# Kernel optimization log

Hardware: AMD Instinct MI355X
Metric: run time of the kernel (lower is better)

The kernel has to match this reference:

```python
import jax, jax.numpy as jnp
import numpy as np

N, T, D, H = 100000, 16, 8, 40
HP1 = H + 1
ALPHA_DP = 1.0
KAPPA0 = 1000.0   # priorGaussianVarKappa
NU0 = 100.0       # priorWishartNu
PSI0_SCALE = 500.0  # priorWishartPsi = 500*I


def setup_inputs() -> dict:
    key = jax.random.key(0)
    ks = jax.random.split(key, 6)
    return {
        "BetaGamma1": jnp.ones((1, T), jnp.float32),
        "Phi": jax.random.uniform(ks[0], (N, T), jnp.float32),
        "inputData": jax.random.normal(ks[1], (N, D), jnp.float32),
        "outputData": jax.random.normal(ks[2], (N, 1), jnp.float32),
        "weightELM": jax.random.uniform(ks[3], (D, H), jnp.float32) * 2.0 - 1.0,
        "biasELM": jax.random.normal(ks[4], (H, 1), jnp.float32),
        "epsilonA": jnp.ones((1, T), jnp.float32),
        "epsilonB": jnp.ones((1, T), jnp.float32),
        "zetaA": 1e-4 * jnp.ones((1, T), jnp.float32),
        "zetaB": jnp.ones((1, T), jnp.float32),
    }


def reference(BetaGamma1, Phi, inputData, outputData, weightELM, biasELM,
              epsilonA, epsilonB, zetaA, zetaB):
    f32 = jnp.float32
    mu0 = jnp.zeros((D, 1), f32)                      # priorGaussianMeanMu
    Psi0 = PSI0_SCALE * jnp.eye(D, dtype=f32)         # priorWishartPsi

    sumPhi = jnp.sum(Phi, axis=0, keepdims=True)      # [1,T]

    # stick-breaking Beta params. Torch builds a flipped [T,N,T] tril mask;
    # mathematically BetaGamma2[t] = alpha + sum_{j>t} sum_n Phi[n,j]
    BetaGamma1_new = jnp.ones_like(BetaGamma1) + sumPhi
    col = sumPhi[0]                                   # [T]
    rev_incl = jnp.cumsum(col[::-1])[::-1]            # sum_{j>=t}
    BetaGamma2 = (ALPHA_DP + (rev_incl - col))[None, :]

    # Gaussian-Wishart natural-parameter updates.
    # Torch loops over clusters doing [N,D,D] bmm outer products; this is
    # S[:,:,t] = sum_n Phi[n,t] x_n x_n^T
    S = jnp.einsum('nt,ni,nj->ijt', Phi, inputData, inputData)  # [D,D,T]
    t11 = -0.5 * (Psi0 + KAPPA0 * mu0 @ mu0.T)[:, :, None] - 0.5 * S
    t12 = KAPPA0 * mu0 + inputData.T @ Phi            # [D,T]
    t21 = -0.5 * sumPhi - 0.5 * (NU0 + D + 2)         # [1,T]
    kappa = KAPPA0 + sumPhi                           # [1,T]
    mu = t12 / kappa                                  # [D,T]
    nu = -2.0 * t21 - 2.0 - float(D)                  # [1,T]
    psi = -2.0 * t11 - kappa[0][None, None, :] * jnp.einsum('it,jt->ijt', mu, mu)

    # ELM feature map + augmented design matrix X = [sigmoid(x W + b), 1]
    hmap = jax.nn.sigmoid(inputData @ weightELM + biasELM.T)   # [N,H]
    X = jnp.concatenate([hmap, jnp.ones((inputData.shape[0], 1), f32)], axis=1)  # [N,HP1]

    epsExp = (epsilonA / epsilonB)[0]                 # [T]
    zetaExp = (zetaA / zetaB)[0]                      # [T]

    # A[t] = X^T diag(Phi[:,t]) X   (torch: per-cluster bmm with diag_embed)
    A = jnp.einsum('nt,ni,nj->tij', Phi, X, X)        # [T,HP1,HP1]
    WS = jnp.linalg.inv(epsExp[:, None, None] * A
                        + zetaExp[:, None, None] * jnp.eye(HP1, dtype=f32))
    # b[t] = X^T diag(Phi[:,t]) y
    b = jnp.einsum('ni,nt->ti', X * outputData, Phi)  # [T,HP1]
    WMv = zetaExp[:, None] * jnp.einsum('tij,tj->ti', WS, b)   # [T,HP1]
    WM = WMv[:, :, None]                              # [T,HP1,1]

    # prior Zeta/Epsilon alias the variational initial values in __init__
    zetaA_new = zetaA + (H + 1) * 0.5
    zetaB_new = zetaB + 0.5 * (jnp.sum(WMv * WMv, axis=1)
                               + jnp.trace(WS, axis1=-2, axis2=-1))[None, :]
    epsA_new = epsilonA + 0.5 * sumPhi

    pred = jnp.einsum('ni,ti->tn', X, WMv)            # [T,N]
    err = outputData.T - pred                          # [T,N]
    t1 = jnp.einsum('tn,nt->t', err * err, Phi)[None, :]
    t2 = jnp.einsum('tij,tji->t', A, WS)[None, :]
    epsB_new = epsilonB + 0.5 * (t1 + t2)

    return (BetaGamma1_new, BetaGamma2, mu, kappa, nu, psi,
            WM, WS, zetaA_new, zetaB_new, epsA_new, epsB_new)
```

## Files before the change

### kernel.cpp

```cpp
#include <hip/hip_runtime.h>

#define Nn 100000
#define Tt 16
#define Dd 8
#define Hh 40
#define HP1 41

#define SPC 8
#define CH  (32 * SPC)
#define KCMAX ((Nn + CH - 1) / CH)

#define NPAIR 1275
#define PSZ (NPAIR * 16)

#define XEH_OFF  0
#define XEL_OFF  (XEH_OFF + 32 * Nn)
#define PHIT_OFF (XEL_OFF + 32 * Nn)
#define PART_OFF (PHIT_OFF + 16 * Nn)
#define P_OFF    (PART_OFF + 8 * PSZ)

#define OFF_BG1   0
#define OFF_BG2   16
#define OFF_MU    32
#define OFF_KAPPA 160
#define OFF_NU    176
#define OFF_PSI   192
#define OFF_WM    1216
#define OFF_WS    1872
#define OFF_ZA    28768
#define OFF_ZB    28784
#define OFF_EA    28800
#define OFF_EB    28816

typedef _Float16 f16x8 __attribute__((ext_vector_type(8)));
typedef float f32x4 __attribute__((ext_vector_type(4)));
typedef unsigned int u32x4 __attribute__((ext_vector_type(4)));

__device__ __forceinline__ int pidx(int i, int j) {
  if (i > j) { int tmp = i; i = j; j = tmp; }
  return (i * (2 * 50 - i + 1)) / 2 + (j - i);
}

__global__ __launch_bounds__(256)
void elm_expand(const float* __restrict__ Phi, const float* __restrict__ Xd,
                const float* __restrict__ Yd, const float* __restrict__ W,
                const float* __restrict__ bb,
                unsigned short* __restrict__ XeHi, unsigned short* __restrict__ XeLo,
                float* __restrict__ PhiT)
{
  __shared__ float sW[Dd * Hh];
  __shared__ float sb[Hh];
  __shared__ float xs[64][9];
  __shared__ float ys[64];
  __shared__ float hrow[64][41];
  __shared__ float pt[16][68];
  int tid = threadIdx.x;
  int n0 = blockIdx.x * 64;

  for (int i = tid; i < Dd * Hh; i += 256) sW[i] = W[i];
  if (tid < Hh) sb[tid] = bb[tid];
  if (tid < 128) {
    int nl = tid >> 1, h4 = (tid & 1) * 4;
    int gn = n0 + nl;
    float4 v = (gn < Nn) ? *(const float4*)(Xd + (size_t)gn * 8 + h4)
                         : make_float4(0.f, 0.f, 0.f, 0.f);
    xs[nl][h4 + 0] = v.x; xs[nl][h4 + 1] = v.y;
    xs[nl][h4 + 2] = v.z; xs[nl][h4 + 3] = v.w;
  }
  if (tid < 64) { int gn = n0 + tid; ys[tid] = (gn < Nn) ? Yd[gn] : 0.f; }
  {
    int nl = tid >> 2, q = tid & 3;
    int gn = n0 + nl;
    float4 v = (gn < Nn) ? *(const float4*)(Phi + (size_t)gn * 16 + q * 4)
                         : make_float4(0.f, 0.f, 0.f, 0.f);
    pt[q * 4 + 0][nl] = v.x; pt[q * 4 + 1][nl] = v.y;
    pt[q * 4 + 2][nl] = v.z; pt[q * 4 + 3][nl] = v.w;
  }
  __syncthreads();
  {
    int nl = tid >> 2, hq = (tid & 3) * 10;
    for (int hh = 0; hh < 10; ++hh) {
      int h = hq + hh;
      float z = sb[h];
#pragma unroll
      for (int d = 0; d < 8; ++d) z = fmaf(xs[nl][d], sW[d * Hh + h], z);
      hrow[nl][h] = 1.f / (1.f + __expf(-z));
    }
  }
  __syncthreads();
  {
    int t = tid & 15, nq = tid >> 4;
    int gn = n0 + nq * 4;
    if (gn < Nn) {
      float4 v = make_float4(pt[t][nq * 4 + 0], pt[t][nq * 4 + 1],
                             pt[t][nq * 4 + 2], pt[t][nq * 4 + 3]);
      *(float4*)(PhiT + (size_t)t * Nn + gn) = v;
    }
  }
  {
    int cidx = tid >> 2, seg = tid & 3;
    int nl0 = seg * 16;
    float vv[16];
#pragma unroll
    for (int j = 0; j < 16; ++j) {
      int n = nl0 + j;
      float v;
      if (cidx < Hh) v = hrow[n][cidx];
      else if (cidx == 40) v = 1.f;
      else if (cidx < 49) v = xs[n][cidx - 41];
      else if (cidx == 49) v = ys[n];
      else v = 0.f;
      vv[j] = v;
    }
    unsigned short hs[16], ls[16];
#pragma unroll
    for (int j = 0; j < 16; ++j) {
      _Float16 h = (_Float16)vv[j];
      float r = vv[j] - (float)h;
      _Float16 lo = (_Float16)r;
      hs[j] = __builtin_bit_cast(unsigned short, h);
      ls[j] = __builtin_bit_cast(unsigned short, lo);
    }
#pragma unroll
    for (int q2 = 0; q2 < 2; ++q2) {
      int gn = n0 + nl0 + q2 * 8;
      if (gn < Nn) {
        uint4 uh, ul;
        uh.x = hs[q2*8+0] | ((unsigned)hs[q2*8+1] << 16);
        uh.y = hs[q2*8+2] | ((unsigned)hs[q2*8+3] << 16);
        uh.z = hs[q2*8+4] | ((unsigned)hs[q2*8+5] << 16);
        uh.w = hs[q2*8+6] | ((unsigned)hs[q2*8+7] << 16);
        ul.x = ls[q2*8+0] | ((unsigned)ls[q2*8+1] << 16);
        ul.y = ls[q2*8+2] | ((unsigned)ls[q2*8+3] << 16);
        ul.z = ls[q2*8+4] | ((unsigned)ls[q2*8+5] << 16);
        ul.w = ls[q2*8+6] | ((unsigned)ls[q2*8+7] << 16);
        *(uint4*)(XeHi + (size_t)cidx * Nn + gn) = uh;
        *(uint4*)(XeLo + (size_t)cidx * Nn + gn) = ul;
      }
    }
  }
}

__device__ __forceinline__ void gload16(const void* g, void* l) {
  __builtin_amdgcn_global_load_lds(
      (const __attribute__((address_space(1))) unsigned int*)g,
      (__attribute__((address_space(3))) unsigned int*)l, 16, 0, 0);
}

#define PHI_LDS 32768
#define LDS_BYTES (PHI_LDS + 16 * CH * 4)

__global__ __launch_bounds__(256, 3)
void gram_mfma(const float* __restrict__ PhiT,
               const unsigned short* __restrict__ XeHi,
               const unsigned short* __restrict__ XeLo,
               float* __restrict__ P, int G)
{
  __shared__ __align__(16) char smem[LDS_BYTES];

  int tid = threadIdx.x;
  int l = tid & 63, w = tid >> 6;
  int l15 = l & 15, lg = l >> 4;
  int bM = blockIdx.x & 3, g = blockIdx.x >> 2;
  int i0 = bM * 13;

  int mbase = (w == 0) ? 0 : (1 + 3 * w);
  int MT = (w == 0) ? 4 : 3;

  int off_b[4];
#pragma unroll
  for (int nt = 0; nt < 4; ++nt) {
    int j = l15 + 16 * nt;
    off_b[nt] = j * 64 + 16 * (lg ^ ((j >> 1) & 3));
  }
  int off_a[4];
#pragma unroll
  for (int mi = 0; mi < 4; ++mi) {
    int i = i0 + mbase + mi;
    off_a[mi] = i * 64 + 16 * (lg ^ ((i >> 1) & 3));
  }
  int off_p0 = PHI_LDS + l15 * 128 + 16 * ((2 * lg) ^ (l15 & 7));
  int off_p1 = PHI_LDS + l15 * 128 + 16 * ((2 * lg + 1) ^ (l15 & 7));

  int srow = tid >> 2;
  int ssl = (tid & 3) ^ ((srow >> 1) & 3);

  f32x4 acc[4][4];
#pragma unroll
  for (int mi = 0; mi < 4; ++mi)
#pragma unroll
    for (int nt = 0; nt < 4; ++nt) acc[mi][nt] = (f32x4){0.f, 0.f, 0.f, 0.f};

  for (int cc = g; cc < KCMAX; cc += G) {
    int n0 = cc * CH;
    int rem = Nn - n0; if (rem > CH) rem = CH;
    int nsteps = rem >> 5;

    __builtin_amdgcn_s_barrier();
    asm volatile("" ::: "memory");

    const char* gH = (const char*)(XeHi + (size_t)srow * Nn + n0 + 8 * ssl);
    const char* gL = (const char*)(XeLo + (size_t)srow * Nn + n0 + 8 * ssl);
#define STAGE(sx) do {                                                    \
    gload16(gH + (size_t)(sx) * 64, &smem[(((sx) & 3) * 8192) + tid * 16]);\
    gload16(gL + (size_t)(sx) * 64,                                       \
            &smem[(((sx) & 3) * 8192) + 4096 + tid * 16]);                \
  } while (0)

#pragma unroll
    for (int q = 0; q < 4; ++q) {
      int gp = tid + q * 256;
      int s = gp >> 7, t = (gp & 127) >> 3, sl = gp & 7;
      int nsrc = n0 + s * 32;
      if (nsrc > Nn - 32) nsrc = Nn - 32;
      gload16(PhiT + (size_t)t * Nn + nsrc + 4 * (sl ^ (t & 7)),
              &smem[PHI_LDS + gp * 16]);
    }
    STAGE(0);
    if (nsteps > 1) STAGE(1);
    if (nsteps > 2) STAGE(2);

    for (int s = 0; s < nsteps; ++s) {
      int out = nsteps - 1 - s; if (out > 2) out = 2;
      if (out == 2)      asm volatile("s_waitcnt vmcnt(4)" ::: "memory");
      else if (out == 1) asm volatile("s_waitcnt vmcnt(2)" ::: "memory");
      else               asm volatile("s_waitcnt vmcnt(0)" ::: "memory");
      __builtin_amdgcn_s_barrier();
      asm volatile("" ::: "memory");
      if (s + 3 < nsteps) STAGE(s + 3);

      const char* base  = &smem[(s & 3) * 8192];
      const char* pbase = &smem[s * 2048];
      f32x4 p0 = *(const f32x4*)(pbase + off_p0);
      f32x4 p1 = *(const f32x4*)(pbase + off_p1);
      float ph[8] = {p0[0], p0[1], p0[2], p0[3], p1[0], p1[1], p1[2], p1[3]};

      f16x8 bh[4], bl[4];
#pragma unroll
      for (int nt = 0; nt < 4; ++nt) {
        bh[nt] = *(const f16x8*)(base + off_b[nt]);
        bl[nt] = *(const f16x8*)(base + 4096 + off_b[nt]);
      }
      __builtin_amdgcn_s_setprio(1);
#pragma unroll
      for (int mi = 0; mi < 4; ++mi) {
        if (mi >= MT) break;
        f16x8 xh = *(const f16x8*)(base + off_a[mi]);
        f16x8 xl = *(const f16x8*)(base + 4096 + off_a[mi]);
        float v0 = ph[0] * ((float)xh[0] + (float)xl[0]);
        float v1 = ph[1] * ((float)xh[1] + (float)xl[1]);
        float v2 = ph[2] * ((float)xh[2] + (float)xl[2]);
        float v3 = ph[3] * ((float)xh[3] + (float)xl[3]);
        float v4 = ph[4] * ((float)xh[4] + (float)xl[4]);
        float v5 = ph[5] * ((float)xh[5] + (float)xl[5]);
        float v6 = ph[6] * ((float)xh[6] + (float)xl[6]);
        float v7 = ph[7] * ((float)xh[7] + (float)xl[7]);
        auto h0 = __builtin_amdgcn_cvt_pkrtz(v0, v1);
        auto h1 = __builtin_amdgcn_cvt_pkrtz(v2, v3);
        auto h2 = __builtin_amdgcn_cvt_pkrtz(v4, v5);
        auto h3 = __builtin_amdgcn_cvt_pkrtz(v6, v7);
        float r0 = v0 - (float)h0[0], r1 = v1 - (float)h0[1];
        float r2 = v2 - (float)h1[0], r3 = v3 - (float)h1[1];
        float r4 = v4 - (float)h2[0], r5 = v5 - (float)h2[1];
        float r6 = v6 - (float)h3[0], r7 = v7 - (float)h3[1];
        auto e0 = __builtin_amdgcn_cvt_pkrtz(r0, r1);
        auto e1 = __builtin_amdgcn_cvt_pkrtz(r2, r3);
        auto e2 = __builtin_amdgcn_cvt_pkrtz(r4, r5);
        auto e3 = __builtin_amdgcn_cvt_pkrtz(r6, r7);
        u32x4 uh = {__builtin_bit_cast(unsigned int, h0), __builtin_bit_cast(unsigned int, h1),
                    __builtin_bit_cast(unsigned int, h2), __builtin_bit_cast(unsigned int, h3)};
        u32x4 ul = {__builtin_bit_cast(unsigned int, e0), __builtin_bit_cast(unsigned int, e1),
                    __builtin_bit_cast(unsigned int, e2), __builtin_bit_cast(unsigned int, e3)};
        f16x8 ah = __builtin_bit_cast(f16x8, uh);
        f16x8 al = __builtin_bit_cast(f16x8, ul);
#pragma unroll
        for (int nt = 0; nt < 4; ++nt) {
          acc[mi][nt] = __builtin_amdgcn_mfma_f32_16x16x32_f16(ah, bh[nt], acc[mi][nt], 0, 0, 0);
          acc[mi][nt] = __builtin_amdgcn_mfma_f32_16x16x32_f16(ah, bl[nt], acc[mi][nt], 0, 0, 0);
          acc[mi][nt] = __builtin_amdgcn_mfma_f32_16x16x32_f16(al, bh[nt], acc[mi][nt], 0, 0, 0);
        }
      }
      __builtin_amdgcn_s_setprio(0);
    }
#undef STAGE
  }

  float* Pc = P + (size_t)g * PSZ;
#pragma unroll
  for (int mi = 0; mi < 4; ++mi) {
    if (mi >= MT) break;
    int i = i0 + mbase + mi;
    if (i < 50) {
#pragma unroll
      for (int nt = 0; nt < 4; ++nt) {
        int j = nt * 16 + l15;
        if (j >= i && j < 50) {
          int pb = (i * (101 - i)) / 2 + (j - i);
          *(f32x4*)(Pc + pb * 16 + lg * 4) = acc[mi][nt];
        }
      }
    }
  }
}

__global__ __launch_bounds__(256)
void reduce_a(const float4* __restrict__ P4, int nslabs, float4* __restrict__ part4)
{
  int g = blockIdx.y;
  int idx = blockIdx.x * 256 + threadIdx.x;
  if (idx >= PSZ / 4) return;
  int per = (nslabs + 7) / 8;
  int c0 = g * per, c1 = c0 + per; if (c1 > nslabs) c1 = nslabs;
  float4 s = make_float4(0.f, 0.f, 0.f, 0.f);
  for (int cc = c0; cc < c1; ++cc) {
    float4 v = P4[(size_t)cc * (PSZ / 4) + idx];
    s.x += v.x; s.y += v.y; s.z += v.z; s.w += v.w;
  }
  part4[(size_t)g * (PSZ / 4) + idx] = s;
}

__device__ __forceinline__ float accv(const float* __restrict__ part, int idx) {
  float s = 0.f;
#pragma unroll
  for (int g = 0; g < 8; ++g) s += part[g * PSZ + idx];
  return s;
}

__global__ __launch_bounds__(256)
void finalize_kernel(const float* __restrict__ part, const float* __restrict__ epsA,
                     const float* __restrict__ epsB, const float* __restrict__ zetA,
                     const float* __restrict__ zetB, float* __restrict__ out)
{
  int t = blockIdx.x;
  int tid = threadIdx.x;
  __shared__ float G[HP1][84];
  __shared__ float As[HP1][HP1 + 1];
  __shared__ float bs[HP1];
  __shared__ float colk[HP1];
  __shared__ float red[256];
  __shared__ float wmv[HP1];
  __shared__ float rowv[4][HP1 + 1];
  __shared__ float mus[Dd];

  float epsExp = epsA[t] / epsB[t];
  float zetaExp = zetA[t] / zetB[t];

  for (int idx = tid; idx < HP1 * HP1; idx += 256) {
    int i = idx / HP1, j = idx % HP1;
    float a = accv(part, pidx(i, j) * Tt + t);
    As[i][j] = a;
    G[i][j] = epsExp * a + (i == j ? zetaExp : 0.f);
    G[i][41 + j] = (i == j) ? 1.f : 0.f;
  }
  for (int idx = tid; idx < HP1; idx += 256) {
    G[idx][82] = 0.f; G[idx][83] = 0.f;
    bs[idx] = accv(part, pidx(idx, 49) * Tt + t);
  }
  __syncthreads();

  int c = tid % HP1;
  int ig = tid / HP1;
  int irow0 = ig * 7;

  for (int k = 0; k < HP1; ++k) {
    float pivinv = 1.f / G[k][k];
    if (tid >= 1 && tid <= HP1) G[k][k + tid] *= pivinv;
    if (tid < HP1) colk[tid] = (tid == k) ? 0.f : G[tid][k];
    __syncthreads();
    if (ig < 6) {
      int j = k + 1 + c;
      float pk = G[k][j];
#pragma unroll
      for (int r = 0; r < 7; ++r) {
        int i = irow0 + r;
        if (i < HP1 && i != k) G[i][j] = fmaf(-colk[i], pk, G[i][j]);
      }
    }
    __syncthreads();
  }

  for (int idx = tid; idx < HP1 * HP1; idx += 256) {
    int i = idx / HP1, j = idx % HP1;
    out[OFF_WS + (t * HP1 + i) * HP1 + j] = G[i][41 + j];
  }
  if (tid < HP1) {
    float s = 0.f;
    for (int j = 0; j < HP1; ++j) s += G[tid][41 + j] * bs[j];
    float w = zetaExp * s;
    wmv[tid] = w;
    out[OFF_WM + t * HP1 + tid] = w;
  }
  __syncthreads();
  float lt2 = 0.f;
  for (int idx = tid; idx < HP1 * HP1; idx += 256) {
    int i = idx / HP1, j = idx % HP1;
    lt2 += As[i][j] * G[i][41 + j];
  }
  red[tid] = lt2; __syncthreads();
  for (int s = 128; s > 0; s >>= 1) {
    if (tid < s) red[tid] += red[tid + s];
    __syncthreads();
  }
  float t2v = red[0];
  if (tid < HP1) {
    float w = wmv[tid];
    float aw = 0.f;
    for (int j = 0; j < HP1; ++j) aw += As[tid][j] * wmv[j];
    rowv[0][tid] = w * bs[tid];
    rowv[1][tid] = w * w;
    rowv[2][tid] = G[tid][41 + tid];
    rowv[3][tid] = w * aw;
  }
  __syncthreads();

  float sp = accv(part, pidx(40, 40) * Tt + t);
  float kap = 1000.f + sp;
  float syy = accv(part, pidx(49, 49) * Tt + t);

  if (tid == 0) {
    float wb = 0.f, wn = 0.f, trc = 0.f, quad = 0.f;
    for (int i = 0; i < HP1; ++i) {
      wb += rowv[0][i]; wn += rowv[1][i]; trc += rowv[2][i]; quad += rowv[3][i];
    }
    float t1 = syy - 2.f * wb + quad;
    out[OFF_BG1 + t] = 1.f + sp;
    float rest = 0.f;
    for (int u = t + 1; u < Tt; ++u) rest += accv(part, pidx(40, 40) * Tt + u);
    out[OFF_BG2 + t] = 1.f + rest;
    out[OFF_KAPPA + t] = kap;
    out[OFF_NU + t] = sp + 100.f;
    out[OFF_ZA + t] = zetA[t] + 0.5f * (float)HP1;
    out[OFF_ZB + t] = zetB[t] + 0.5f * (wn + trc);
    out[OFF_EA + t] = epsA[t] + 0.5f * sp;
    out[OFF_EB + t] = epsB[t] + 0.5f * (t1 + t2v);
  }
  if (tid < Dd) {
    float m = accv(part, pidx(40, 41 + tid) * Tt + t) / kap;
    mus[tid] = m;
    out[OFF_MU + tid * Tt + t] = m;
  }
  __syncthreads();
  if (tid < Dd * Dd) {
    int i = tid / Dd, j = tid % Dd;
    float S = accv(part, pidx(41 + i, 41 + j) * Tt + t);
    float v = (i == j ? 500.f : 0.f) + S - kap * mus[i] * mus[j];
    out[OFF_PSI + (i * Dd + j) * Tt + t] = v;
  }
}

extern "C" void kernel_launch(void* const* d_in, const int* in_sizes, int n_in,
                              void* d_out, int out_size, void* d_ws, size_t ws_size,
                              hipStream_t stream) {
  const float* Phi = (const float*)d_in[1];
  const float* Xd  = (const float*)d_in[2];
  const float* Yd  = (const float*)d_in[3];
  const float* W   = (const float*)d_in[4];
  const float* bb  = (const float*)d_in[5];
  const float* eA  = (const float*)d_in[6];
  const float* eB  = (const float*)d_in[7];
  const float* zA  = (const float*)d_in[8];
  const float* zB  = (const float*)d_in[9];
  float* out = (float*)d_out;
  float* ws  = (float*)d_ws;

  unsigned short* XeHi = (unsigned short*)(ws + XEH_OFF);
  unsigned short* XeLo = (unsigned short*)(ws + XEL_OFF);
  float* PhiT = ws + PHIT_OFF;
  float* part = ws + PART_OFF;
  float* P    = ws + P_OFF;

  long maxSlabs = ((long)(ws_size / 4) - (long)P_OFF) / PSZ;
  int G = (int)(maxSlabs < KCMAX ? maxSlabs : KCMAX);
  if (G < 1) G = 1;

  hipLaunchKernelGGL(elm_expand, dim3((Nn + 63) / 64), dim3(256), 0, stream,
                     Phi, Xd, Yd, W, bb, XeHi, XeLo, PhiT);
  hipLaunchKernelGGL(gram_mfma, dim3(4 * G), dim3(256), 0, stream,
                     PhiT, XeHi, XeLo, P, G);
  hipLaunchKernelGGL(reduce_a, dim3(20, 8), dim3(256), 0, stream,
                     (const float4*)P, G, (float4*)part);
  hipLaunchKernelGGL(finalize_kernel, dim3(Tt), dim3(256), 0, stream,
                     part, eA, eB, zA, zB, out);
}
```

Before: 183.9 us.

## Drop LDS staging in gram kernel and remap blocks for L2 locality

Removes the async global-to-LDS staging pipeline (global_load_lds, barriers, swizzled LDS offsets) and has each wave load its A, B and Phi fragments directly from global memory. It also remaps block indices so the four row-blocks sharing a chunk group are eight blocks apart, and pads the grid to a multiple of eight, presumably so different XCDs or the L2 can share chunk data. This removes barrier and LDS overhead but relies on cache hits for the repeated fragment loads. It also loses the explicit prefetch overlap, so memory latency may be exposed.

```diff
diff --git a/kernel.cpp b/kernel.cpp
--- a/kernel.cpp
+++ b/kernel.cpp
@@ -141,112 +141,59 @@
   }
 }
 
-__device__ __forceinline__ void gload16(const void* g, void* l) {
-  __builtin_amdgcn_global_load_lds(
-      (const __attribute__((address_space(1))) unsigned int*)g,
-      (__attribute__((address_space(3))) unsigned int*)l, 16, 0, 0);
-}
-
-#define PHI_LDS 32768
-#define LDS_BYTES (PHI_LDS + 16 * CH * 4)
-
 __global__ __launch_bounds__(256, 3)
 void gram_mfma(const float* __restrict__ PhiT,
                const unsigned short* __restrict__ XeHi,
                const unsigned short* __restrict__ XeLo,
                float* __restrict__ P, int G)
 {
-  __shared__ __align__(16) char smem[LDS_BYTES];
-
   int tid = threadIdx.x;
   int l = tid & 63, w = tid >> 6;
   int l15 = l & 15, lg = l >> 4;
-  int bM = blockIdx.x & 3, g = blockIdx.x >> 2;
+
+  int id = blockIdx.x;
+  int bM = (id >> 3) & 3;
+  int g = (id & 7) | ((id >> 5) << 3);
+  if (g >= G) return;
   int i0 = bM * 13;
 
   int mbase = (w == 0) ? 0 : (1 + 3 * w);
   int MT = (w == 0) ? 4 : 3;
 
-  int off_b[4];
-#pragma unroll
-  for (int nt = 0; nt < 4; ++nt) {
-    int j = l15 + 16 * nt;
-    off_b[nt] = j * 64 + 16 * (lg ^ ((j >> 1) & 3));
-  }
-  int off_a[4];
-#pragma unroll
-  for (int mi = 0; mi < 4; ++mi) {
-    int i = i0 + mbase + mi;
-    off_a[mi] = i * 64 + 16 * (lg ^ ((i >> 1) & 3));
-  }
-  int off_p0 = PHI_LDS + l15 * 128 + 16 * ((2 * lg) ^ (l15 & 7));
-  int off_p1 = PHI_LDS + l15 * 128 + 16 * ((2 * lg + 1) ^ (l15 & 7));
-
-  int srow = tid >> 2;
-  int ssl = (tid & 3) ^ ((srow >> 1) & 3);
-
   f32x4 acc[4][4];
 #pragma unroll
   for (int mi = 0; mi < 4; ++mi)
 #pragma unroll
     for (int nt = 0; nt < 4; ++nt) acc[mi][nt] = (f32x4){0.f, 0.f, 0.f, 0.f};
+
+  const float* prow = PhiT + (size_t)l15 * Nn;
 
   for (int cc = g; cc < KCMAX; cc += G) {
     int n0 = cc * CH;
     int rem = Nn - n0; if (rem > CH) rem = CH;
     int nsteps = rem >> 5;
 
-    __builtin_amdgcn_s_barrier();
-    asm volatile("" ::: "memory");
-
-    const char* gH = (const char*)(XeHi + (size_t)srow * Nn + n0 + 8 * ssl);
-    const char* gL = (const char*)(XeLo + (size_t)srow * Nn + n0 + 8 * ssl);
-#define STAGE(sx) do {                                                    \
-    gload16(gH + (size_t)(sx) * 64, &smem[(((sx) & 3) * 8192) + tid * 16]);\
-    gload16(gL + (size_t)(sx) * 64,                                       \
-            &smem[(((sx) & 3) * 8192) + 4096 + tid * 16]);                \
-  } while (0)
-
-#pragma unroll
-    for (int q = 0; q < 4; ++q) {
-      int gp = tid + q * 256;
-      int s = gp >> 7, t = (gp & 127) >> 3, sl = gp & 7;
-      int nsrc = n0 + s * 32;
-      if (nsrc > Nn - 32) nsrc = Nn - 32;
-      gload16(PhiT + (size_t)t * Nn + nsrc + 4 * (sl ^ (t & 7)),
-              &smem[PHI_LDS + gp * 16]);
-    }
-    STAGE(0);
-    if (nsteps > 1) STAGE(1);
-    if (nsteps > 2) STAGE(2);
-
     for (int s = 0; s < nsteps; ++s) {
-      int out = nsteps - 1 - s; if (out > 2) out = 2;
-      if (out == 2)      asm volatile("s_waitcnt vmcnt(4)" ::: "memory");
-      else if (out == 1) asm volatile("s_waitcnt vmcnt(2)" ::: "memory");
-      else               asm volatile("s_waitcnt vmcnt(0)" ::: "memory");
-      __builtin_amdgcn_s_barrier();
-      asm volatile("" ::: "memory");
-      if (s + 3 < nsteps) STAGE(s + 3);
-
-      const char* base  = &smem[(s & 3) * 8192];
-      const char* pbase = &smem[s * 2048];
-      f32x4 p0 = *(const f32x4*)(pbase + off_p0);
-      f32x4 p1 = *(const f32x4*)(pbase + off_p1);
+      int kb = n0 + s * 32 + lg * 8;
+
+      f32x4 p0 = *(const f32x4*)(prow + kb);
+      f32x4 p1 = *(const f32x4*)(prow + kb + 4);
       float ph[8] = {p0[0], p0[1], p0[2], p0[3], p1[0], p1[1], p1[2], p1[3]};
 
       f16x8 bh[4], bl[4];
 #pragma unroll
       for (int nt = 0; nt < 4; ++nt) {
-        bh[nt] = *(const f16x8*)(base + off_b[nt]);
-        bl[nt] = *(const f16x8*)(base + 4096 + off_b[nt]);
+        int j = l15 + 16 * nt;
+        bh[nt] = *(const f16x8*)(XeHi + (size_t)j * Nn + kb);
+        bl[nt] = *(const f16x8*)(XeLo + (size_t)j * Nn + kb);
       }
       __builtin_amdgcn_s_setprio(1);
 #pragma unroll
       for (int mi = 0; mi < 4; ++mi) {
         if (mi >= MT) break;
-        f16x8 xh = *(const f16x8*)(base + off_a[mi]);
-        f16x8 xl = *(const f16x8*)(base + 4096 + off_a[mi]);
+        int i = i0 + mbase + mi;
+        f16x8 xh = *(const f16x8*)(XeHi + (size_t)i * Nn + kb);
+        f16x8 xl = *(const f16x8*)(XeLo + (size_t)i * Nn + kb);
         float v0 = ph[0] * ((float)xh[0] + (float)xl[0]);
         float v1 = ph[1] * ((float)xh[1] + (float)xl[1]);
         float v2 = ph[2] * ((float)xh[2] + (float)xl[2]);
@@ -282,7 +229,6 @@
       }
       __builtin_amdgcn_s_setprio(0);
     }
-#undef STAGE
   }
 
   float* Pc = P + (size_t)g * PSZ;
@@ -472,10 +418,11 @@
   long maxSlabs = ((long)(ws_size / 4) - (long)P_OFF) / PSZ;
   int G = (int)(maxSlabs < KCMAX ? maxSlabs : KCMAX);
   if (G < 1) G = 1;
+  int Gpad = ((G + 7) / 8) * 8;
 
   hipLaunchKernelGGL(elm_expand, dim3((Nn + 63) / 64), dim3(256), 0, stream,
                      Phi, Xd, Yd, W, bb, XeHi, XeLo, PhiT);
-  hipLaunchKernelGGL(gram_mfma, dim3(4 * G), dim3(256), 0, stream,
+  hipLaunchKernelGGL(gram_mfma, dim3(4 * Gpad), dim3(256), 0, stream,
                      PhiT, XeHi, XeLo, P, G);
   hipLaunchKernelGGL(reduce_a, dim3(20, 8), dim3(256), 0, stream,
                      (const float4*)P, G, (float4*)part);
```

Result: slower. 206.7 us (+12.4%).

## Split Gram rows into two halves per block and stream fp32 A operand

Applied to the files above, without the earlier changes.

Each gram block now covers 26 rows (two row-halves instead of four quarters), with up to 7 m-tiles per wave, so each staged B chunk is reused across more rows and fewer blocks reload the same XeHi/XeLo data. The A operand is read from a new fp32 copy of the expanded features written by elm_expand and staged into LDS, rather than rebuilt from the hi+lo fp16 pair. Block IDs are remapped so the two halves of a slab are interleaved, and occupancy drops to 2 blocks per SM because of the larger accumulators and LDS. This costs an extra fp32 write in elm_expand and more global traffic per stage.

```diff
diff --git a/kernel.cpp b/kernel.cpp
--- a/kernel.cpp
+++ b/kernel.cpp
@@ -15,7 +15,8 @@
 
 #define XEH_OFF  0
 #define XEL_OFF  (XEH_OFF + 32 * Nn)
-#define PHIT_OFF (XEL_OFF + 32 * Nn)
+#define XEF_OFF  (XEL_OFF + 32 * Nn)
+#define PHIT_OFF (XEF_OFF + 64 * Nn)
 #define PART_OFF (PHIT_OFF + 16 * Nn)
 #define P_OFF    (PART_OFF + 8 * PSZ)
 
@@ -46,7 +47,7 @@
                 const float* __restrict__ Yd, const float* __restrict__ W,
                 const float* __restrict__ bb,
                 unsigned short* __restrict__ XeHi, unsigned short* __restrict__ XeLo,
-                float* __restrict__ PhiT)
+                float* __restrict__ XeF32, float* __restrict__ PhiT)
 {
   __shared__ float sW[Dd * Hh];
   __shared__ float sb[Hh];
@@ -111,6 +112,13 @@
       else if (cidx == 49) v = ys[n];
       else v = 0.f;
       vv[j] = v;
+    }
+#pragma unroll
+    for (int q2 = 0; q2 < 4; ++q2) {
+      int gn = n0 + nl0 + q2 * 4;
+      if (gn < Nn)
+        *(float4*)(XeF32 + (size_t)cidx * Nn + gn) =
+            make_float4(vv[q2 * 4], vv[q2 * 4 + 1], vv[q2 * 4 + 2], vv[q2 * 4 + 3]);
     }
     unsigned short hs[16], ls[16];
 #pragma unroll
@@ -147,13 +155,15 @@
       (__attribute__((address_space(3))) unsigned int*)l, 16, 0, 0);
 }
 
-#define PHI_LDS 32768
+#define AF_LDS  32768
+#define PHI_LDS 49152
 #define LDS_BYTES (PHI_LDS + 16 * CH * 4)
 
-__global__ __launch_bounds__(256, 3)
+__global__ __launch_bounds__(256, 2)
 void gram_mfma(const float* __restrict__ PhiT,
                const unsigned short* __restrict__ XeHi,
                const unsigned short* __restrict__ XeLo,
+               const float* __restrict__ XeF32,
                float* __restrict__ P, int G)
 {
   __shared__ __align__(16) char smem[LDS_BYTES];
@@ -161,11 +171,15 @@
   int tid = threadIdx.x;
   int l = tid & 63, w = tid >> 6;
   int l15 = l & 15, lg = l >> 4;
-  int bM = blockIdx.x & 3, g = blockIdx.x >> 2;
-  int i0 = bM * 13;
-
-  int mbase = (w == 0) ? 0 : (1 + 3 * w);
-  int MT = (w == 0) ? 4 : 3;
+
+  int id = blockIdx.x;
+  int h = (id >> 3) & 1;
+  int g = (id & 7) | ((id >> 4) << 3);
+  if (g >= G) return;
+  int i0 = h * 26;
+
+  int MT = (w < 2) ? 7 : 6;
+  int mbase = (w < 2) ? 7 * w : 14 + 6 * (w - 2);
 
   int off_b[4];
 #pragma unroll
@@ -173,21 +187,20 @@
     int j = l15 + 16 * nt;
     off_b[nt] = j * 64 + 16 * (lg ^ ((j >> 1) & 3));
   }
-  int off_a[4];
-#pragma unroll
-  for (int mi = 0; mi < 4; ++mi) {
-    int i = i0 + mbase + mi;
-    off_a[mi] = i * 64 + 16 * (lg ^ ((i >> 1) & 3));
-  }
+  int afoff[7];
+#pragma unroll
+  for (int mi = 0; mi < 7; ++mi)
+    afoff[mi] = (mbase + mi) * 128 + lg * 32;
   int off_p0 = PHI_LDS + l15 * 128 + 16 * ((2 * lg) ^ (l15 & 7));
   int off_p1 = PHI_LDS + l15 * 128 + 16 * ((2 * lg + 1) ^ (l15 & 7));
 
   int srow = tid >> 2;
   int ssl = (tid & 3) ^ ((srow >> 1) & 3);
-
-  f32x4 acc[4][4];
-#pragma unroll
-  for (int mi = 0; mi < 4; ++mi)
+  int arow = tid >> 3, aslot = tid & 7;
+
+  f32x4 acc[7][4];
+#pragma unroll
+  for (int mi = 0; mi < 7; ++mi)
 #pragma unroll
     for (int nt = 0; nt < 4; ++nt) acc[mi][nt] = (f32x4){0.f, 0.f, 0.f, 0.f};
 
@@ -201,10 +214,13 @@
 
     const char* gH = (const char*)(XeHi + (size_t)srow * Nn + n0 + 8 * ssl);
     const char* gL = (const char*)(XeLo + (size_t)srow * Nn + n0 + 8 * ssl);
-#define STAGE(sx) do {                                                    \
-    gload16(gH + (size_t)(sx) * 64, &smem[(((sx) & 3) * 8192) + tid * 16]);\
-    gload16(gL + (size_t)(sx) * 64,                                       \
-            &smem[(((sx) & 3) * 8192) + 4096 + tid * 16]);                \
+    const char* gA = (const char*)(XeF32 + (size_t)(i0 + arow) * Nn + n0 + 4 * aslot);
+#define STAGE(sx) do {                                                     \
+    gload16(gH + (size_t)(sx) * 64, &smem[(((sx) & 3) * 8192) + tid * 16]); \
+    gload16(gL + (size_t)(sx) * 64,                                        \
+            &smem[(((sx) & 3) * 8192) + 4096 + tid * 16]);                 \
+    gload16(gA + (size_t)(sx) * 128,                                       \
+            &smem[AF_LDS + (((sx) & 3) * 4096) + tid * 16]);               \
   } while (0)
 
 #pragma unroll
@@ -222,14 +238,15 @@
 
     for (int s = 0; s < nsteps; ++s) {
       int out = nsteps - 1 - s; if (out > 2) out = 2;
-      if (out == 2)      asm volatile("s_waitcnt vmcnt(4)" ::: "memory");
-      else if (out == 1) asm volatile("s_waitcnt vmcnt(2)" ::: "memory");
+      if (out == 2)      asm volatile("s_waitcnt vmcnt(6)" ::: "memory");
+      else if (out == 1) asm volatile("s_waitcnt vmcnt(3)" ::: "memory");
       else               asm volatile("s_waitcnt vmcnt(0)" ::: "memory");
       __builtin_amdgcn_s_barrier();
       asm volatile("" ::: "memory");
       if (s + 3 < nsteps) STAGE(s + 3);
 
       const char* base  = &smem[(s & 3) * 8192];
+      const char* abase = &smem[AF_LDS + (s & 3) * 4096];
       const char* pbase = &smem[s * 2048];
       f32x4 p0 = *(const f32x4*)(pbase + off_p0);
       f32x4 p1 = *(const f32x4*)(pbase + off_p1);
@@ -243,18 +260,14 @@
       }
       __builtin_amdgcn_s_setprio(1);
 #pragma unroll
-      for (int mi = 0; mi < 4; ++mi) {
+      for (int mi = 0; mi < 7; ++mi) {
         if (mi >= MT) break;
-        f16x8 xh = *(const f16x8*)(base + off_a[mi]);
-        f16x8 xl = *(const f16x8*)(base + 4096 + off_a[mi]);
-        float v0 = ph[0] * ((float)xh[0] + (float)xl[0]);
-        float v1 = ph[1] * ((float)xh[1] + (float)xl[1]);
-        float v2 = ph[2] * ((float)xh[2] + (float)xl[2]);
-        float v3 = ph[3] * ((float)xh[3] + (float)xl[3]);
-        float v4 = ph[4] * ((float)xh[4] + (float)xl[4]);
-        float v5 = ph[5] * ((float)xh[5] + (float)xl[5]);
-        float v6 = ph[6] * ((float)xh[6] + (float)xl[6]);
-        float v7 = ph[7] * ((float)xh[7] + (float)xl[7]);
+        f32x4 xa0 = *(const f32x4*)(abase + afoff[mi]);
+        f32x4 xa1 = *(const f32x4*)(abase + afoff[mi] + 16);
+        float v0 = ph[0] * xa0[0], v1 = ph[1] * xa0[1];
+        float v2 = ph[2] * xa0[2], v3 = ph[3] * xa0[3];
+        float v4 = ph[4] * xa1[0], v5 = ph[5] * xa1[1];
+        float v6 = ph[6] * xa1[2], v7 = ph[7] * xa1[3];
         auto h0 = __builtin_amdgcn_cvt_pkrtz(v0, v1);
         auto h1 = __builtin_amdgcn_cvt_pkrtz(v2, v3);
         auto h2 = __builtin_amdgcn_cvt_pkrtz(v4, v5);
@@ -287,7 +300,7 @@
 
   float* Pc = P + (size_t)g * PSZ;
 #pragma unroll
-  for (int mi = 0; mi < 4; ++mi) {
+  for (int mi = 0; mi < 7; ++mi) {
     if (mi >= MT) break;
     int i = i0 + mbase + mi;
     if (i < 50) {
@@ -465,18 +478,20 @@
 
   unsigned short* XeHi = (unsigned short*)(ws + XEH_OFF);
   unsigned short* XeLo = (unsigned short*)(ws + XEL_OFF);
-  float* PhiT = ws + PHIT_OFF;
-  float* part = ws + PART_OFF;
-  float* P    = ws + P_OFF;
+  float* XeF32 = ws + XEF_OFF;
+  float* PhiT  = ws + PHIT_OFF;
+  float* part  = ws + PART_OFF;
+  float* P     = ws + P_OFF;
 
   long maxSlabs = ((long)(ws_size / 4) - (long)P_OFF) / PSZ;
   int G = (int)(maxSlabs < KCMAX ? maxSlabs : KCMAX);
   if (G < 1) G = 1;
+  int Gpad = ((G + 7) / 8) * 8;
 
   hipLaunchKernelGGL(elm_expand, dim3((Nn + 63) / 64), dim3(256), 0, stream,
-                     Phi, Xd, Yd, W, bb, XeHi, XeLo, PhiT);
-  hipLaunchKernelGGL(gram_mfma, dim3(4 * G), dim3(256), 0, stream,
-                     PhiT, XeHi, XeLo, P, G);
+                     Phi, Xd, Yd, W, bb, XeHi, XeLo, XeF32, PhiT);
+  hipLaunchKernelGGL(gram_mfma, dim3(2 * Gpad), dim3(256), 0, stream,
+                     PhiT, XeHi, XeLo, XeF32, P, G);
   hipLaunchKernelGGL(reduce_a, dim3(20, 8), dim3(256), 0, stream,
                      (const float4*)P, G, (float4*)part);
   hipLaunchKernelGGL(finalize_kernel, dim3(Tt), dim3(256), 0, stream,
```

Result: no change. 185.3 us (+0.7%).
